# Performance work log

Hardware: AMD Instinct MI355X
Metric: run time of the kernel (lower is better)

The kernel has to match this reference:

```python
import jax, jax.numpy as jnp
import numpy as np

DIM = 512
WS = 8
NH = 16
HD = DIM // NH
N = WS * WS
B = 2048
SCALE = HD ** -0.5


def _rel_pos_index(ws):
    # Swin relative position index for a ws x ws window -> [N*N] int indices
    coords = np.stack(np.meshgrid(np.arange(ws), np.arange(ws), indexing='ij')).reshape(2, -1)
    rel = coords[:, :, None] - coords[:, None, :]          # [2, N, N]
    rel = rel.transpose(1, 2, 0).copy()                    # [N, N, 2]
    rel[..., 0] += ws - 1
    rel[..., 1] += ws - 1
    rel[..., 0] *= 2 * ws - 1
    return rel.sum(-1).reshape(-1)                         # [N*N]

REL_IDX = jnp.asarray(_rel_pos_index(WS))


def setup_inputs() -> dict:
    key = jax.random.key(0)
    ks = jax.random.split(key, 6)
    x = jax.random.normal(ks[0], (B, N, DIM), dtype=jnp.float32)
    W_qkv = jax.random.normal(ks[1], (3 * DIM, DIM), dtype=jnp.float32) * 0.02
    b_qkv = jnp.zeros((3 * DIM,), dtype=jnp.float32)
    W_proj = jax.random.normal(ks[2], (DIM, DIM), dtype=jnp.float32) * 0.02
    b_proj = jnp.zeros((DIM,), dtype=jnp.float32)
    bias_table = jax.random.normal(ks[3], ((2 * WS - 1) * (2 * WS - 1), NH), dtype=jnp.float32) * 0.02
    return {"x": x, "W_qkv": W_qkv, "b_qkv": b_qkv, "W_proj": W_proj, "b_proj": b_proj, "bias_table": bias_table}


def reference(x, W_qkv, b_qkv, W_proj, b_proj, bias_table):
    B_, n, c = x.shape
    qkv = x @ W_qkv.T + b_qkv                              # [B, N, 3C]
    qkv = qkv.reshape(B_, n, 3, NH, HD)
    q = qkv[:, :, 0].transpose(0, 2, 1, 3)                 # [B, H, N, hd]
    k = qkv[:, :, 1].transpose(0, 2, 1, 3)
    v = qkv[:, :, 2].transpose(0, 2, 1, 3)
    attn = jnp.einsum('bhnd,bhmd->bhnm', q, k) * SCALE     # [B, H, N, N]
    bias = bias_table[REL_IDX].reshape(n, n, NH).transpose(2, 0, 1)  # [H, N, N]
    attn = jax.nn.softmax(attn + bias[None], axis=-1)
    out = jnp.einsum('bhnm,bhmd->bhnd', attn, v)           # [B, H, N, hd]
    out = out.transpose(0, 2, 1, 3).reshape(B_, n, c)      # [B, N, C]
    return out @ W_proj.T + b_proj
```

## Files before the change

### kernel.cpp

```cpp
#include <hip/hip_runtime.h>
#include <stdint.h>

#define NHEADS 16
#define HDIM 32
#define NTOK 64
#define NWIN_B 2048
#define MROWS (NWIN_B * NTOK)
#define CDIM 512
#define QKVDIM 1536
#define ATT_SCALE 0.17677669529663687f

typedef __attribute__((ext_vector_type(8))) short short8;
typedef __attribute__((ext_vector_type(4))) float f32x4;

__device__ __forceinline__ unsigned short f2bf(float f) {
  unsigned int u = __float_as_uint(f);
  u += 0x7FFFu + ((u >> 16) & 1u);
  return (unsigned short)(u >> 16);
}

__device__ __forceinline__ void gload_lds16(const unsigned short* g, unsigned short* l) {
  __builtin_amdgcn_global_load_lds(
      (const __attribute__((address_space(1))) unsigned int*)g,
      (__attribute__((address_space(3))) unsigned int*)l, 16, 0, 0);
}

__global__ void cvt_bf16_kernel(const float* __restrict__ src,
                                unsigned short* __restrict__ dst, int n4) {
  int i = blockIdx.x * blockDim.x + threadIdx.x;
  if (i >= n4) return;
  const float4 v = ((const float4*)src)[i];
  ushort4 o;
  o.x = f2bf(v.x); o.y = f2bf(v.y); o.z = f2bf(v.z); o.w = f2bf(v.w);
  ((ushort4*)dst)[i] = o;
}

__global__ void expand_bias_kernel(const float* __restrict__ table,
                                   float* __restrict__ biasx) {
  const int t = blockIdx.x * blockDim.x + threadIdx.x;
  const int col = t & 63, row = (t >> 6) & 63, h = t >> 12;
  const int idx = ((row >> 3) - (col >> 3) + 7) * 15 + ((row & 7) - (col & 7) + 7);
  biasx[t] = table[idx * NHEADS + h];
}

template <typename OutT>
__global__ __launch_bounds__(256) void gemm_bt_kernel(
    const unsigned short* __restrict__ A,
    const unsigned short* __restrict__ Bt,
    const float* __restrict__ bias,
    OutT* __restrict__ C, int M, int N, int K, int nxb) {
  constexpr int BM = 128, BN = 128, BK = 64;
  __shared__ __align__(16) unsigned short smem[BM * BK + BN * BK];
  unsigned short* As = smem;
  unsigned short* Bs = smem + BM * BK;

  const int tid = threadIdx.x;
  const int w = tid >> 6, lane = tid & 63;
  const int quad = lane >> 4, l16 = lane & 15;
  const int wr = w >> 1, wc = w & 1;

  const int nyb_per_xcd = (gridDim.x / nxb) >> 3;
  const int xcd = blockIdx.x & 7;
  const int idx = blockIdx.x >> 3;
  const long rowBase = (long)(xcd * nyb_per_xcd + idx / nxb) * BM;
  const long colBase = (long)(idx % nxb) * BN;

  const int srow8 = lane >> 3;
  const int gchunk = (lane & 7) ^ srow8;

  const long aBase0 = (rowBase + w * 32 + srow8) * (long)K + gchunk * 8;
  const long bBase0 = (colBase + w * 32 + srow8) * (long)K + gchunk * 8;

  f32x4 acc[4][4] = {};

  for (int k0 = 0; k0 < K; k0 += BK) {
#pragma unroll
    for (int i = 0; i < 4; ++i) {
      gload_lds16(A  + aBase0 + (long)(i * 8) * K + k0, &As[(w * 32 + i * 8) * BK]);
      gload_lds16(Bt + bBase0 + (long)(i * 8) * K + k0, &Bs[(w * 32 + i * 8) * BK]);
    }
    __syncthreads();
#pragma unroll
    for (int kkc = 0; kkc < 2; ++kkc) {
      const int p = ((quad + kkc * 4) ^ (l16 & 7)) * 8;
      short8 aF[4], bF[4];
#pragma unroll
      for (int t = 0; t < 4; ++t)
        aF[t] = *(const short8*)&As[(wr * 64 + t * 16 + l16) * BK + p];
#pragma unroll
      for (int t = 0; t < 4; ++t)
        bF[t] = *(const short8*)&Bs[(wc * 64 + t * 16 + l16) * BK + p];
#pragma unroll
      for (int mt = 0; mt < 4; ++mt)
#pragma unroll
        for (int nt = 0; nt < 4; ++nt)
          acc[mt][nt] = __builtin_amdgcn_mfma_f32_16x16x32_bf16(
              aF[mt], bF[nt], acc[mt][nt], 0, 0, 0);
    }
    __syncthreads();
  }

  if constexpr (sizeof(OutT) == 2) {
    unsigned short* Cs = smem;
#pragma unroll
    for (int nt = 0; nt < 4; ++nt) {
      const int col = wc * 64 + nt * 16 + l16;
      const float bv = bias[colBase + col];
#pragma unroll
      for (int mt = 0; mt < 4; ++mt) {
        const int row0 = wr * 64 + mt * 16 + quad * 4;
#pragma unroll
        for (int r = 0; r < 4; ++r)
          Cs[(row0 + r) * 128 + col] = f2bf(acc[mt][nt][r] + bv);
      }
    }
    __syncthreads();
#pragma unroll
    for (int t = 0; t < 8; ++t) {
      const int ci = t * 256 + tid;
      const int row = ci >> 4, ch = ci & 15;
      *(short8*)((unsigned short*)C + (rowBase + row) * N + colBase + ch * 8) =
          *(const short8*)&Cs[ci * 8];
    }
  } else {
#pragma unroll
    for (int nt = 0; nt < 4; ++nt) {
      const long col = colBase + wc * 64 + nt * 16 + l16;
      const float bv = bias[col];
#pragma unroll
      for (int mt = 0; mt < 4; ++mt) {
        const long row0 = rowBase + wr * 64 + mt * 16 + quad * 4;
#pragma unroll
        for (int r = 0; r < 4; ++r)
          C[(row0 + r) * N + col] = acc[mt][nt][r] + bv;
      }
    }
  }
}

__global__ __launch_bounds__(256) void attn_kernel(
    const unsigned short* __restrict__ qkv,
    const float* __restrict__ biasx,
    unsigned short* __restrict__ aout) {
  __shared__ __align__(16) unsigned short sT[3 * 64 * 128];
  unsigned short* P = sT;

  const int tid = threadIdx.x;
  const int w = tid >> 6, lane = tid & 63;
  const int quad = lane >> 4, l16 = lane & 15;
  const int b = blockIdx.x >> 2;
  const int q = blockIdx.x & 3;
  const int h = q * 4 + w;

  const unsigned short* base = qkv + (long)b * NTOK * QKVDIM + q * 128;

  const int rloc = lane >> 4;
  const int ch = lane & 15;
#pragma unroll
  for (int t = 0; t < 3; ++t) {
#pragma unroll
    for (int i = 0; i < 4; ++i) {
      const int r = w * 16 + i * 4 + rloc;
      const int gc = ch ^ (r & 15);
      gload_lds16(base + (long)r * QKVDIM + t * 512 + gc * 8,
                  &sT[t * 8192 + (w * 16 + i * 4) * 128]);
    }
  }
  __syncthreads();

  short8 qF[4], kF[4];
  const int pQ = ((w * 4 + quad) ^ l16) * 8;
#pragma unroll
  for (int t = 0; t < 4; ++t) {
    qF[t] = *(const short8*)&sT[0 * 8192 + (t * 16 + l16) * 128 + pQ];
    kF[t] = *(const short8*)&sT[1 * 8192 + (t * 16 + l16) * 128 + pQ];
  }

  f32x4 S[4][4];
#pragma unroll
  for (int mi = 0; mi < 4; ++mi)
#pragma unroll
    for (int ni = 0; ni < 4; ++ni) {
      f32x4 z = {0.f, 0.f, 0.f, 0.f};
      S[mi][ni] = __builtin_amdgcn_mfma_f32_16x16x32_bf16(qF[mi], kF[ni], z, 0, 0, 0);
    }

  short8 vF[2][2];
#pragma unroll
  for (int kt = 0; kt < 2; ++kt)
#pragma unroll
    for (int dt = 0; dt < 2; ++dt) {
      short8 f;
#pragma unroll
      for (int j = 0; j < 8; ++j) {
        const int n = kt * 32 + quad * 8 + j;
        const int c = w * 4 + dt * 2 + (l16 >> 3);
        f[j] = (short)sT[2 * 8192 + n * 128 + (c ^ (n & 15)) * 8 + (l16 & 7)];
      }
      vF[kt][dt] = f;
    }

  __syncthreads();

  const float* bh = biasx + h * (NTOK * NTOK);
#pragma unroll
  for (int mi = 0; mi < 4; ++mi) {
#pragma unroll
    for (int r = 0; r < 4; ++r) {
      const int row = mi * 16 + quad * 4 + r;
      float vals[4], mx = -3.4e38f;
#pragma unroll
      for (int ni = 0; ni < 4; ++ni) {
        const float s = S[mi][ni][r] * ATT_SCALE + bh[row * 64 + ni * 16 + l16];
        vals[ni] = s;
        mx = fmaxf(mx, s);
      }
#pragma unroll
      for (int d = 1; d < 16; d <<= 1) mx = fmaxf(mx, __shfl_xor(mx, d));
      float sum = 0.f;
#pragma unroll
      for (int ni = 0; ni < 4; ++ni) { vals[ni] = __expf(vals[ni] - mx); sum += vals[ni]; }
#pragma unroll
      for (int d = 1; d < 16; d <<= 1) sum += __shfl_xor(sum, d);
      const float inv = 1.0f / sum;
#pragma unroll
      for (int ni = 0; ni < 4; ++ni)
        P[w * 4608 + row * 72 + ni * 16 + l16] = f2bf(vals[ni] * inv);
    }
  }

  f32x4 O[4][2] = {};
#pragma unroll
  for (int mi = 0; mi < 4; ++mi)
#pragma unroll
    for (int kt = 0; kt < 2; ++kt) {
      const short8 pF = *(const short8*)&P[w * 4608 + (mi * 16 + l16) * 72 + kt * 32 + quad * 8];
#pragma unroll
      for (int dt = 0; dt < 2; ++dt)
        O[mi][dt] = __builtin_amdgcn_mfma_f32_16x16x32_bf16(pF, vF[kt][dt], O[mi][dt], 0, 0, 0);
    }

#pragma unroll
  for (int mi = 0; mi < 4; ++mi)
#pragma unroll
    for (int dt = 0; dt < 2; ++dt)
#pragma unroll
      for (int r = 0; r < 4; ++r) {
        const int row = mi * 16 + quad * 4 + r;
        aout[((long)b * NTOK + row) * CDIM + h * HDIM + dt * 16 + l16] = f2bf(O[mi][dt][r]);
      }
}

extern "C" void kernel_launch(void* const* d_in, const int* in_sizes, int n_in,
                              void* d_out, int out_size, void* d_ws, size_t ws_size,
                              hipStream_t stream) {
  const float* x      = (const float*)d_in[0];
  const float* W_qkv  = (const float*)d_in[1];
  const float* b_qkv  = (const float*)d_in[2];
  const float* W_proj = (const float*)d_in[3];
  const float* b_proj = (const float*)d_in[4];
  const float* btab   = (const float*)d_in[5];

  char* ws = (char*)d_ws;
  unsigned short* qkv   = (unsigned short*)ws;
  unsigned short* xb    = (unsigned short*)(ws + 402653184L);
  unsigned short* aout  = xb;
  unsigned short* wqkvb = (unsigned short*)(ws + 402653184L + 134217728L);
  unsigned short* wprjb = (unsigned short*)(ws + 402653184L + 134217728L + 1572864L);
  float*          biasx = (float*)(ws + 402653184L + 134217728L + 1572864L + 524288L);

  cvt_bf16_kernel<<<(MROWS * CDIM) / 1024, 256, 0, stream>>>(x, xb, (MROWS * CDIM) / 4);
  cvt_bf16_kernel<<<(QKVDIM * CDIM) / 1024, 256, 0, stream>>>(W_qkv, wqkvb, (QKVDIM * CDIM) / 4);
  cvt_bf16_kernel<<<(CDIM * CDIM) / 1024, 256, 0, stream>>>(W_proj, wprjb, (CDIM * CDIM) / 4);
  expand_bias_kernel<<<(NHEADS * NTOK * NTOK) / 256, 256, 0, stream>>>(btab, biasx);

  gemm_bt_kernel<unsigned short><<<(MROWS / 128) * (QKVDIM / 128), 256, 0, stream>>>(
      xb, wqkvb, b_qkv, qkv, MROWS, QKVDIM, CDIM, QKVDIM / 128);

  attn_kernel<<<NWIN_B * 4, 256, 0, stream>>>(qkv, biasx, aout);

  gemm_bt_kernel<float><<<(MROWS / 128) * (CDIM / 128), 256, 0, stream>>>(
      aout, wprjb, b_proj, (float*)d_out, MROWS, CDIM, CDIM, CDIM / 128);
}
```

Before: 1.015 ms.

## Replace GEMMs with 256x256 double-buffered 8-wave pipelined kernel

Both projection GEMMs move from a 128x128 single-buffered, 4-wave tile to a 256x256 tile with 8 waves and double-buffered LDS. Global-to-LDS loads for the next K step are interleaved with MFMA quadrants, using explicit waitcnt, barriers and setprio to overlap memory with compute. The larger tile raises operand reuse and cuts global traffic per FLOP. In exchange it uses 128KB of LDS and many accumulator registers, and the hand-placed barrier and waitcnt sequence is fragile.

```diff
diff --git a/kernel.cpp b/kernel.cpp
--- a/kernel.cpp
+++ b/kernel.cpp
@@ -43,96 +43,170 @@
   biasx[t] = table[idx * NHEADS + h];
 }
 
+
+#define MMAQ(qm, qn)                                                          \
+  do {                                                                        \
+    _Pragma("unroll") for (int kk = 0; kk < 2; ++kk)                          \
+    _Pragma("unroll") for (int mt = 0; mt < 4; ++mt)                          \
+    _Pragma("unroll") for (int nt = 0; nt < 2; ++nt)                          \
+      acc[(qm) * 4 + mt][(qn) * 2 + nt] =                                     \
+          __builtin_amdgcn_mfma_f32_16x16x32_bf16(                            \
+              aF[mt][kk], bF[(qn) * 2 + nt][kk],                              \
+              acc[(qm) * 4 + mt][(qn) * 2 + nt], 0, 0, 0);                    \
+  } while (0)
+
+#define LDB_Q(buf, qn)                                                        \
+  do {                                                                        \
+    _Pragma("unroll") for (int nt = 0; nt < 2; ++nt) {                        \
+      const int rb_ = wn * 64 + ((qn) * 2 + nt) * 16 + l16;                   \
+      _Pragma("unroll") for (int kk = 0; kk < 2; ++kk) {                      \
+        const int pb_ = ((kk * 4 + quad) ^ (l16 & 7)) * 8;                    \
+        bF[(qn) * 2 + nt][kk] =                                               \
+            *(const short8*)&lds[(buf) * BUFSZ + ATILE + rb_ * 64 + pb_];     \
+      }                                                                       \
+    }                                                                         \
+  } while (0)
+
 template <typename OutT>
-__global__ __launch_bounds__(256) void gemm_bt_kernel(
+__global__ __launch_bounds__(512, 2) void gemm256_kernel(
     const unsigned short* __restrict__ A,
     const unsigned short* __restrict__ Bt,
     const float* __restrict__ bias,
     OutT* __restrict__ C, int M, int N, int K, int nxb) {
-  constexpr int BM = 128, BN = 128, BK = 64;
-  __shared__ __align__(16) unsigned short smem[BM * BK + BN * BK];
-  unsigned short* As = smem;
-  unsigned short* Bs = smem + BM * BK;
+  constexpr int BK = 64;
+  constexpr int ATILE = 256 * BK;
+  constexpr int BUFSZ = 2 * ATILE;
+  __shared__ __align__(16) unsigned short lds[2 * BUFSZ];
 
   const int tid = threadIdx.x;
   const int w = tid >> 6, lane = tid & 63;
   const int quad = lane >> 4, l16 = lane & 15;
-  const int wr = w >> 1, wc = w & 1;
+  const int wm = w >> 2, wn = w & 3;
+  const int srow8 = lane >> 3, gch = (lane & 7) ^ srow8;
 
   const int nyb_per_xcd = (gridDim.x / nxb) >> 3;
   const int xcd = blockIdx.x & 7;
   const int idx = blockIdx.x >> 3;
-  const long rowBase = (long)(xcd * nyb_per_xcd + idx / nxb) * BM;
-  const long colBase = (long)(idx % nxb) * BN;
-
-  const int srow8 = lane >> 3;
-  const int gchunk = (lane & 7) ^ srow8;
-
-  const long aBase0 = (rowBase + w * 32 + srow8) * (long)K + gchunk * 8;
-  const long bBase0 = (colBase + w * 32 + srow8) * (long)K + gchunk * 8;
-
-  f32x4 acc[4][4] = {};
-
-  for (int k0 = 0; k0 < K; k0 += BK) {
-#pragma unroll
-    for (int i = 0; i < 4; ++i) {
-      gload_lds16(A  + aBase0 + (long)(i * 8) * K + k0, &As[(w * 32 + i * 8) * BK]);
-      gload_lds16(Bt + bBase0 + (long)(i * 8) * K + k0, &Bs[(w * 32 + i * 8) * BK]);
+  const long rowBase = (long)(xcd * nyb_per_xcd + idx / nxb) * 256;
+  const long colBase = (long)(idx % nxb) * 256;
+  const int NT = K / BK;
+
+  const unsigned short* aSrc = A + (rowBase + w * 8 + srow8) * (long)K + gch * 8;
+  const unsigned short* bSrc = Bt + (colBase + w * 8 + srow8) * (long)K + gch * 8;
+
+  auto stageA = [&](int buf, int half, int kt) {
+    unsigned short* dst = &lds[buf * BUFSZ + (half * 128 + w * 8) * BK];
+    const unsigned short* src = aSrc + (long)half * 128 * K + kt * BK;
+    gload_lds16(src, dst);
+    gload_lds16(src + 64 * (long)K, dst + 64 * BK);
+  };
+  auto stageB = [&](int buf, int half, int kt) {
+    unsigned short* dst = &lds[buf * BUFSZ + ATILE + (half * 128 + w * 8) * BK];
+    const unsigned short* src = bSrc + (long)half * 128 * K + kt * BK;
+    gload_lds16(src, dst);
+    gload_lds16(src + 64 * (long)K, dst + 64 * BK);
+  };
+
+  f32x4 acc[8][4] = {};
+  short8 aF[4][2], bF[4][2];
+
+  auto ldA = [&](int buf, int qm) {
+#pragma unroll
+    for (int mt = 0; mt < 4; ++mt) {
+      const int r = wm * 128 + qm * 64 + mt * 16 + l16;
+#pragma unroll
+      for (int kk = 0; kk < 2; ++kk) {
+        const int p = ((kk * 4 + quad) ^ (l16 & 7)) * 8;
+        aF[mt][kk] = *(const short8*)&lds[buf * BUFSZ + r * 64 + p];
+      }
+    }
+  };
+
+  stageA(0, 0, 0); stageA(0, 1, 0); stageB(0, 0, 0); stageB(0, 1, 0);
+  if (NT > 1) { stageB(1, 0, 1); stageB(1, 1, 1); }
+  asm volatile("s_waitcnt vmcnt(4)" ::: "memory");
+  __builtin_amdgcn_s_barrier();
+
+  for (int u = 0; u < NT; ++u) {
+    const int cur = u & 1, nxt = cur ^ 1;
+
+    ldA(cur, 0);
+    LDB_Q(cur, 0);
+    if (u + 1 < NT) stageA(nxt, 0, u + 1);
+    asm volatile("s_waitcnt lgkmcnt(8)" ::: "memory");
+    __builtin_amdgcn_s_barrier();
+    asm volatile("s_waitcnt lgkmcnt(0)" ::: "memory");
+    __builtin_amdgcn_sched_barrier(0);
+    __builtin_amdgcn_s_setprio(1);
+    MMAQ(0, 0);
+    __builtin_amdgcn_s_setprio(0);
+    __builtin_amdgcn_s_barrier();
+
+    LDB_Q(cur, 1);
+    if (u + 1 < NT) stageA(nxt, 1, u + 1);
+    __builtin_amdgcn_s_barrier();
+    asm volatile("s_waitcnt lgkmcnt(0)" ::: "memory");
+    __builtin_amdgcn_sched_barrier(0);
+    __builtin_amdgcn_s_setprio(1);
+    MMAQ(0, 1);
+    __builtin_amdgcn_s_setprio(0);
+    __builtin_amdgcn_s_barrier();
+
+    ldA(cur, 1);
+    if (u + 2 < NT) stageB(cur, 0, u + 2);
+    __builtin_amdgcn_s_barrier();
+    asm volatile("s_waitcnt lgkmcnt(0)" ::: "memory");
+    __builtin_amdgcn_sched_barrier(0);
+    __builtin_amdgcn_s_setprio(1);
+    MMAQ(1, 1);
+    __builtin_amdgcn_s_setprio(0);
+    __builtin_amdgcn_s_barrier();
+
+    if (u + 2 < NT) stageB(cur, 1, u + 2);
+    __builtin_amdgcn_s_barrier();
+    __builtin_amdgcn_s_setprio(1);
+    MMAQ(1, 0);
+    __builtin_amdgcn_s_setprio(0);
+    if (u + 1 < NT) {
+      if (u + 2 < NT) asm volatile("s_waitcnt vmcnt(4)" ::: "memory");
+      else            asm volatile("s_waitcnt vmcnt(0)" ::: "memory");
+    }
+    __builtin_amdgcn_s_barrier();
+  }
+
+  if constexpr (sizeof(OutT) == 2) {
+    unsigned short* Cs = &lds[0];
+#pragma unroll
+    for (int ni = 0; ni < 4; ++ni) {
+      const int col = wn * 64 + ni * 16 + l16;
+      const float bv = bias[colBase + col];
+#pragma unroll
+      for (int mi = 0; mi < 8; ++mi) {
+        const int row0 = wm * 128 + mi * 16 + quad * 4;
+#pragma unroll
+        for (int r = 0; r < 4; ++r)
+          Cs[(row0 + r) * 256 + col] = f2bf(acc[mi][ni][r] + bv);
+      }
     }
     __syncthreads();
 #pragma unroll
-    for (int kkc = 0; kkc < 2; ++kkc) {
-      const int p = ((quad + kkc * 4) ^ (l16 & 7)) * 8;
-      short8 aF[4], bF[4];
-#pragma unroll
-      for (int t = 0; t < 4; ++t)
-        aF[t] = *(const short8*)&As[(wr * 64 + t * 16 + l16) * BK + p];
-#pragma unroll
-      for (int t = 0; t < 4; ++t)
-        bF[t] = *(const short8*)&Bs[(wc * 64 + t * 16 + l16) * BK + p];
-#pragma unroll
-      for (int mt = 0; mt < 4; ++mt)
-#pragma unroll
-        for (int nt = 0; nt < 4; ++nt)
-          acc[mt][nt] = __builtin_amdgcn_mfma_f32_16x16x32_bf16(
-              aF[mt], bF[nt], acc[mt][nt], 0, 0, 0);
-    }
-    __syncthreads();
-  }
-
-  if constexpr (sizeof(OutT) == 2) {
-    unsigned short* Cs = smem;
-#pragma unroll
-    for (int nt = 0; nt < 4; ++nt) {
-      const int col = wc * 64 + nt * 16 + l16;
-      const float bv = bias[colBase + col];
-#pragma unroll
-      for (int mt = 0; mt < 4; ++mt) {
-        const int row0 = wr * 64 + mt * 16 + quad * 4;
-#pragma unroll
-        for (int r = 0; r < 4; ++r)
-          Cs[(row0 + r) * 128 + col] = f2bf(acc[mt][nt][r] + bv);
-      }
-    }
-    __syncthreads();
-#pragma unroll
-    for (int t = 0; t < 8; ++t) {
-      const int ci = t * 256 + tid;
-      const int row = ci >> 4, ch = ci & 15;
+    for (int t = 0; t < 16; ++t) {
+      const int ci = t * 512 + tid;
+      const int row = ci >> 5, ch = ci & 31;
       *(short8*)((unsigned short*)C + (rowBase + row) * N + colBase + ch * 8) =
           *(const short8*)&Cs[ci * 8];
     }
   } else {
 #pragma unroll
-    for (int nt = 0; nt < 4; ++nt) {
-      const long col = colBase + wc * 64 + nt * 16 + l16;
+    for (int ni = 0; ni < 4; ++ni) {
+      const long col = colBase + wn * 64 + ni * 16 + l16;
       const float bv = bias[col];
 #pragma unroll
-      for (int mt = 0; mt < 4; ++mt) {
-        const long row0 = rowBase + wr * 64 + mt * 16 + quad * 4;
+      for (int mi = 0; mi < 8; ++mi) {
+        const long row0 = rowBase + wm * 128 + mi * 16 + quad * 4;
 #pragma unroll
         for (int r = 0; r < 4; ++r)
-          C[(row0 + r) * N + col] = acc[mt][nt][r] + bv;
+          C[(row0 + r) * N + col] = acc[mi][ni][r] + bv;
       }
     }
   }
@@ -274,11 +348,11 @@
   cvt_bf16_kernel<<<(CDIM * CDIM) / 1024, 256, 0, stream>>>(W_proj, wprjb, (CDIM * CDIM) / 4);
   expand_bias_kernel<<<(NHEADS * NTOK * NTOK) / 256, 256, 0, stream>>>(btab, biasx);
 
-  gemm_bt_kernel<unsigned short><<<(MROWS / 128) * (QKVDIM / 128), 256, 0, stream>>>(
-      xb, wqkvb, b_qkv, qkv, MROWS, QKVDIM, CDIM, QKVDIM / 128);
+  gemm256_kernel<unsigned short><<<(MROWS / 256) * (QKVDIM / 256), 512, 0, stream>>>(
+      xb, wqkvb, b_qkv, qkv, MROWS, QKVDIM, CDIM, QKVDIM / 256);
 
   attn_kernel<<<NWIN_B * 4, 256, 0, stream>>>(qkv, biasx, aout);
 
-  gemm_bt_kernel<float><<<(MROWS / 128) * (CDIM / 128), 256, 0, stream>>>(
-      aout, wprjb, b_proj, (float*)d_out, MROWS, CDIM, CDIM, CDIM / 128);
-}
+  gemm256_kernel<float><<<(MROWS / 256) * (CDIM / 256), 512, 0, stream>>>(
+      aout, wprjb, b_proj, (float*)d_out, MROWS, CDIM, CDIM, CDIM / 256);
+}
```

Result: faster. 943.8 us (-7.1%).
